# Kernel optimization log

Hardware: AMD Instinct MI355X
Metric: run time of the kernel (lower is better)

The kernel has to match this reference:

```python
import jax, jax.numpy as jnp
import numpy as np

D = 512; H = 8; DH = D // H; FFN = 2048; K = 31; N = 4; T = 1024


def _ln(x, g, b):
    m = jnp.mean(x, -1, keepdims=True)
    v = jnp.var(x, -1, keepdims=True)
    return (x - m) * jax.lax.rsqrt(v + 1e-5) * g + b


def _ff(x, g, b, w1, b1, w2, b2):
    h = jax.nn.silu(_ln(x, g, b) @ w1 + b1)
    return 0.5 * (h @ w2 + b2)


def _forward(x, rel_pe, ln1_g, ln1_b, ff1_w1, ff1_b1, ff1_w2, ff1_b2,
             an_g, an_b, wq, bq, wk, bk, wv, bv, wo, bo, pos_w, u, v,
             cn_g, cn_b, pe_w, pe_b, dw_w, dw_b, bn_g, bn_b, pc_w, pc_b,
             ln2_g, ln2_b, ff2_w1, ff2_b1, ff2_w2, ff2_b2, fn_g, fn_b):
    Nb, Tt, _ = x.shape
    # macaron FF 1 (half-step)
    x = x + _ff(x, ln1_g, ln1_b, ff1_w1, ff1_b1, ff1_w2, ff1_b2)

    # RPE multi-head attention (Transformer-XL style)
    xa = _ln(x, an_g, an_b)
    split = lambda m: m.reshape(Nb, Tt, H, DH).transpose(0, 2, 1, 3)  # (N,H,T,dh)
    Q = split(xa @ wq + bq)
    Kk = split(xa @ wk + bk)
    V = split(xa @ wv + bv)
    # content-to-content: (Q+u) K^T
    AC = jnp.einsum('nhtd,nhsd->nhts', Q + u[None, :, None, :], Kk)
    # content-to-position: (Q+v) R^T, then rel-shift gather
    R = (rel_pe @ pos_w).reshape(2 * Tt - 1, H, DH)  # (2T-1,H,dh)
    BD_raw = jnp.einsum('nhtd,phd->nhtp', Q + v[None, :, None, :], R)  # (N,H,T,2T-1)
    idx = jnp.arange(Tt - 1, -1, -1)[None, :] + jnp.arange(Tt)[:, None]  # (T,T): i-j+(T-1)
    BD = jnp.take_along_axis(BD_raw, idx[None, None, :, :], axis=-1)  # (N,H,T,T)
    scores = (AC + BD) * (DH ** -0.5)
    attn = jax.nn.softmax(scores, axis=-1)
    out = jnp.einsum('nhts,nhsd->nthd', attn, V).reshape(Nb, Tt, D)
    x = x + (out @ wo + bo)

    # conv module: LN -> pointwise expand -> GLU -> depthwise conv -> BN(eval) -> SiLU -> pointwise
    c = _ln(x, cn_g, cn_b) @ pe_w + pe_b  # (N,T,2D)
    a, g = jnp.split(c, 2, axis=-1)
    c = a * jax.nn.sigmoid(g)
    c = c.transpose(0, 2, 1)  # (N,D,T)
    c = jax.lax.conv_general_dilated(
        c, dw_w, window_strides=(1,), padding=[(K // 2, K // 2)],
        dimension_numbers=('NCH', 'OIH', 'NCH'), feature_group_count=D)
    c = c + dw_b[None, :, None]
    # BatchNorm1d in eval mode: running_mean=0, running_var=1
    c = c * bn_g[None, :, None] + bn_b[None, :, None]
    c = jax.nn.silu(c).transpose(0, 2, 1) @ pc_w + pc_b
    x = x + c

    # macaron FF 2 + final LN
    x = x + _ff(x, ln2_g, ln2_b, ff2_w1, ff2_b1, ff2_w2, ff2_b2)
    return _ln(x, fn_g, fn_b)


def setup_inputs() -> dict:
    keys = iter(jax.random.split(jax.random.key(0), 64))
    def rn(*shape, s=0.02):
        return jax.random.normal(next(keys), shape, jnp.float32) * s
    inp = {}
    inp['x'] = rn(N, T, D, s=1.0)
    inp['rel_pe'] = rn(2 * T - 1, D, s=1.0)
    inp['ln1_g'] = jnp.ones(D); inp['ln1_b'] = jnp.zeros(D)
    inp['ff1_w1'] = rn(D, FFN); inp['ff1_b1'] = jnp.zeros(FFN)
    inp['ff1_w2'] = rn(FFN, D); inp['ff1_b2'] = jnp.zeros(D)
    inp['an_g'] = jnp.ones(D); inp['an_b'] = jnp.zeros(D)
    inp['wq'] = rn(D, D); inp['bq'] = jnp.zeros(D)
    inp['wk'] = rn(D, D); inp['bk'] = jnp.zeros(D)
    inp['wv'] = rn(D, D); inp['bv'] = jnp.zeros(D)
    inp['wo'] = rn(D, D); inp['bo'] = jnp.zeros(D)
    inp['pos_w'] = rn(D, D)
    inp['u'] = rn(H, DH); inp['v'] = rn(H, DH)
    inp['cn_g'] = jnp.ones(D); inp['cn_b'] = jnp.zeros(D)
    inp['pe_w'] = rn(D, 2 * D); inp['pe_b'] = jnp.zeros(2 * D)
    inp['dw_w'] = rn(D, 1, K); inp['dw_b'] = jnp.zeros(D)
    inp['bn_g'] = jnp.ones(D); inp['bn_b'] = jnp.zeros(D)
    inp['pc_w'] = rn(D, D); inp['pc_b'] = jnp.zeros(D)
    inp['ln2_g'] = jnp.ones(D); inp['ln2_b'] = jnp.zeros(D)
    inp['ff2_w1'] = rn(D, FFN); inp['ff2_b1'] = jnp.zeros(FFN)
    inp['ff2_w2'] = rn(FFN, D); inp['ff2_b2'] = jnp.zeros(D)
    inp['fn_g'] = jnp.ones(D); inp['fn_b'] = jnp.zeros(D)
    return inp


def reference(x, rel_pe, ln1_g, ln1_b, ff1_w1, ff1_b1, ff1_w2, ff1_b2,
              an_g, an_b, wq, bq, wk, bk, wv, bv, wo, bo, pos_w, u, v,
              cn_g, cn_b, pe_w, pe_b, dw_w, dw_b, bn_g, bn_b, pc_w, pc_b,
              ln2_g, ln2_b, ff2_w1, ff2_b1, ff2_w2, ff2_b2, fn_g, fn_b):
    return _forward(x, rel_pe, ln1_g, ln1_b, ff1_w1, ff1_b1, ff1_w2, ff1_b2,
                    an_g, an_b, wq, bq, wk, bk, wv, bv, wo, bo, pos_w, u, v,
                    cn_g, cn_b, pe_w, pe_b, dw_w, dw_b, bn_g, bn_b, pc_w, pc_b,
                    ln2_g, ln2_b, ff2_w1, ff2_b1, ff2_w2, ff2_b2, fn_g, fn_b)
```

## Files before the change

### kernel.cpp

```cpp
#include <hip/hip_runtime.h>
#include <hip/hip_bf16.h>

using bf16 = __hip_bfloat16;
typedef __attribute__((ext_vector_type(8))) short short8;
typedef __attribute__((ext_vector_type(4))) float f32x4;

static __device__ __forceinline__ float b2f(bf16 v) { return __bfloat162float(v); }
static __device__ __forceinline__ bf16  f2b(float v) { return __float2bfloat16(v); }
static __device__ __forceinline__ short f2bs(float x) {
    union { float f; unsigned u; } c; c.f = x;
    unsigned r = (c.u + 0x7FFFu + ((c.u >> 16) & 1u)) >> 16;
    return (short)r;
}
static __device__ __forceinline__ float bs2f(short s) {
    union { unsigned u; float f; } c; c.u = ((unsigned)(unsigned short)s) << 16;
    return c.f;
}
static __device__ __forceinline__ void gload16(const short* g, short* l) {
    __builtin_amdgcn_global_load_lds(
        (const __attribute__((address_space(1))) void*)g,
        (__attribute__((address_space(3))) void*)l, 16, 0, 0);
}

constexpr int kD   = 512;
constexpr int kT   = 1024;
constexpr int kN   = 4;
constexpr int kH   = 8;
constexpr int kDH  = 64;
constexpr int kFFN = 2048;
constexpr int kROWS = kN * kT;
constexpr int kP    = 2 * kT - 1;

#define ACT_NONE 0
#define ACT_SILU 1

__global__ __launch_bounds__(256) void stamp_kernel(float* __restrict__ out, int n, float val) {
    int i = blockIdx.x * 256 + threadIdx.x;
    if (i < n) out[i] = (i == 0 ? val : 0.f);
}

__global__ __launch_bounds__(256) void cvt_kernel(const float* __restrict__ in,
                                                  float* __restrict__ out, int n4) {
    int i = blockIdx.x * 256 + threadIdx.x;
    if (i < n4) ((f32x4*)out)[i] = ((const f32x4*)in)[i];
}

struct WtDesc { const float* src; short* dst; int K; int N; int tstart; };
struct WtArgs { WtDesc d[11]; };

__global__ __launch_bounds__(256) void wt_all_kernel(WtArgs a) {
    __shared__ float t[32][33];
    int bid = blockIdx.x;
    int i = 0;
#pragma unroll
    for (int j = 1; j < 11; ++j) if (bid >= a.d[j].tstart) i = j;
    const float* W = a.d[i].src;
    short* Wt = a.d[i].dst;
    int Kd = a.d[i].K, Nd = a.d[i].N;
    int lt = bid - a.d[i].tstart;
    int nx = Nd >> 5;
    int n0 = (lt % nx) * 32, k0 = (lt / nx) * 32;
    int tx = threadIdx.x & 31, ty = threadIdx.x >> 5;
#pragma unroll
    for (int it = 0; it < 4; ++it)
        t[ty + it * 8][tx] = W[(size_t)(k0 + ty + it * 8) * Nd + n0 + tx];
    __syncthreads();
#pragma unroll
    for (int it = 0; it < 4; ++it)
        Wt[(size_t)(n0 + ty + it * 8) * Kd + k0 + tx] = f2bs(t[tx][ty + it * 8]);
}

__global__ __launch_bounds__(256) void vtrans_kernel(const bf16* __restrict__ V,
                                                     bf16* __restrict__ Vt) {
    __shared__ short ts[64][72];
    int tt = blockIdx.x, h = blockIdx.y, n = blockIdx.z;
    int tid = threadIdx.x;
    int r = tid >> 3, cg = (tid & 7) * 8;
#pragma unroll
    for (int it = 0; it < 2; ++it) {
        int row = it * 32 + r;
        *(short8*)&ts[row][cg] =
            *(const short8*)((const short*)V + ((size_t)n * kT + tt * 64 + row) * 512 + h * 64 + cg);
    }
    __syncthreads();
#pragma unroll
    for (int it = 0; it < 2; ++it) {
        int d = it * 32 + r;
        short8 o;
#pragma unroll
        for (int i = 0; i < 8; ++i) o[i] = ts[cg + i][d];
        *(short8*)((short*)Vt + ((size_t)(n * 8 + h) * 64 + d) * 1024 + tt * 64 + cg) = o;
    }
}

__global__ __launch_bounds__(256) void dwt_kernel(const float* __restrict__ dw_w,
                                                  const float* __restrict__ dw_b,
                                                  const float* __restrict__ bn_g,
                                                  const float* __restrict__ bn_b,
                                                  float* __restrict__ wt,
                                                  float* __restrict__ beff) {
    int idx = blockIdx.x * 256 + threadIdx.x;
    if (idx < 31 * kD) {
        int d = idx & 511, k = idx >> 9;
        wt[k * kD + d] = dw_w[d * 31 + k] * bn_g[d];
    }
    if (idx < kD) beff[idx] = dw_b[idx] * bn_g[idx] + bn_b[idx];
}

__global__ __launch_bounds__(256) void ln_kernel(const float* __restrict__ xin,
                                                 const float* __restrict__ g,
                                                 const float* __restrict__ b,
                                                 void* __restrict__ outp, int out_f32) {
    int row = blockIdx.x;
    const float* xr = xin + (size_t)row * kD;
    int tid = threadIdx.x;
    float v0 = xr[tid], v1 = xr[tid + 256];
    float s = v0 + v1, sq = v0 * v0 + v1 * v1;
    for (int off = 32; off; off >>= 1) {
        s  += __shfl_down(s, off);
        sq += __shfl_down(sq, off);
    }
    __shared__ float ss[4], ssq[4];
    __shared__ float mean_s, rstd_s;
    int wid = tid >> 6, lane = tid & 63;
    if (lane == 0) { ss[wid] = s; ssq[wid] = sq; }
    __syncthreads();
    if (tid == 0) {
        float S  = ss[0] + ss[1] + ss[2] + ss[3];
        float SQ = ssq[0] + ssq[1] + ssq[2] + ssq[3];
        float m = S / (float)kD;
        float var = SQ / (float)kD - m * m;
        mean_s = m;
        rstd_s = rsqrtf(fmaxf(var, 0.f) + 1e-5f);
    }
    __syncthreads();
    float m = mean_s, rs = rstd_s;
    float o0 = (v0 - m) * rs * g[tid]       + b[tid];
    float o1 = (v1 - m) * rs * g[tid + 256] + b[tid + 256];
    size_t i0 = (size_t)row * kD + tid, i1 = i0 + 256;
    if (out_f32) {
        ((float*)outp)[i0] = o0; ((float*)outp)[i1] = o1;
    } else {
        ((bf16*)outp)[i0] = f2b(o0); ((bf16*)outp)[i1] = f2b(o1);
    }
}

__global__ __launch_bounds__(256, 4) void gemm_mfma64(
    const void* __restrict__ A, const short* __restrict__ Bt,
    const float* __restrict__ bias, const float* __restrict__ residual,
    float* __restrict__ outf, bf16* __restrict__ outb,
    int M, int N, int K, int act, float scale, int a_f32) {
    __shared__ short As[4096];
    __shared__ short Bs[4096];
    int tid = threadIdx.x;
    int m0 = blockIdx.y * 64, n0 = blockIdx.x * 64;
    int wid = tid >> 6, lane = tid & 63;
    int wm = (wid >> 1) * 32, wn = (wid & 1) * 32;
    int q = lane >> 4, c16 = lane & 15;

    f32x4 zero4 = {0.f, 0.f, 0.f, 0.f};
    f32x4 acc[2][2] = {{zero4, zero4}, {zero4, zero4}};

    int arow = lane >> 3;
    int aseg = (lane & 7) ^ arow;

    for (int k0 = 0; k0 < K; k0 += 64) {
        __syncthreads();
        if (!a_f32) {
#pragma unroll
            for (int it = 0; it < 2; ++it) {
                int rbase = (wid * 2 + it) * 8;
                gload16((const short*)A + (size_t)(m0 + rbase + arow) * K + k0 + aseg * 8,
                        As + (size_t)(wid * 2 + it) * 512);
            }
        } else {
            int srow = tid >> 3, sseg = tid & 7;
#pragma unroll
            for (int it = 0; it < 2; ++it) {
                int row = it * 32 + srow;
                int rr = m0 + row;
                short8 v = {0, 0, 0, 0, 0, 0, 0, 0};
                if (rr < M) {
                    const float* ap = (const float*)A + (size_t)rr * K + k0 + sseg * 8;
                    f32x4 x0 = *(const f32x4*)ap;
                    f32x4 x1 = *(const f32x4*)(ap + 4);
                    v[0] = f2bs(x0[0]); v[1] = f2bs(x0[1]); v[2] = f2bs(x0[2]); v[3] = f2bs(x0[3]);
                    v[4] = f2bs(x1[0]); v[5] = f2bs(x1[1]); v[6] = f2bs(x1[2]); v[7] = f2bs(x1[3]);
                }
                *(short8*)&As[(row * 8 + (sseg ^ (row & 7))) * 8] = v;
            }
        }
#pragma unroll
        for (int it = 0; it < 2; ++it) {
            int rbase = (wid * 2 + it) * 8;
            gload16(Bt + (size_t)(n0 + rbase + arow) * K + k0 + aseg * 8,
                    Bs + (size_t)(wid * 2 + it) * 512);
        }
        __syncthreads();
#pragma unroll
        for (int ks = 0; ks < 2; ++ks) {
            int p = c16 & 7;
            short8 af[2], bfr[2];
#pragma unroll
            for (int mt = 0; mt < 2; ++mt) {
                int row = wm + mt * 16 + c16;
                af[mt] = *(const short8*)&As[(row * 8 + ((ks * 4 + q) ^ p)) * 8];
            }
#pragma unroll
            for (int nt = 0; nt < 2; ++nt) {
                int row = wn + nt * 16 + c16;
                bfr[nt] = *(const short8*)&Bs[(row * 8 + ((ks * 4 + q) ^ p)) * 8];
            }
#pragma unroll
            for (int mt = 0; mt < 2; ++mt)
#pragma unroll
                for (int nt = 0; nt < 2; ++nt)
                    acc[mt][nt] = __builtin_amdgcn_mfma_f32_16x16x32_bf16(
                        af[mt], bfr[nt], acc[mt][nt], 0, 0, 0);
        }
    }
#pragma unroll
    for (int mt = 0; mt < 2; ++mt) {
#pragma unroll
        for (int reg = 0; reg < 4; ++reg) {
            int r = m0 + wm + mt * 16 + q * 4 + reg;
            if (r >= M) continue;
#pragma unroll
            for (int nt = 0; nt < 2; ++nt) {
                int c = n0 + wn + nt * 16 + c16;
                float h = acc[mt][nt][reg];
                if (bias) h += bias[c];
                if (act == ACT_SILU) h = h / (1.f + __expf(-h));
                h *= scale;
                size_t idx = (size_t)r * N + c;
                if (residual) h += residual[idx];
                if (outf) outf[idx] = h;
                if (outb) outb[idx] = f2b(h);
            }
        }
    }
}

__global__ __launch_bounds__(256, 4) void gemm_qkv(
    const bf16* __restrict__ A, const short* __restrict__ Bt,
    const float* __restrict__ bq, const float* __restrict__ bk,
    const float* __restrict__ bv,
    bf16* __restrict__ Qb, bf16* __restrict__ Kb, bf16* __restrict__ Vb) {
    const int K = kD;
    __shared__ short As[4096];
    __shared__ short Bs[4096];
    int tid = threadIdx.x;
    int m0 = blockIdx.y * 64, n0 = blockIdx.x * 64;
    int seg = blockIdx.x >> 3;
    const float* bias = seg == 0 ? bq : (seg == 1 ? bk : bv);
    bf16* outb = seg == 0 ? Qb : (seg == 1 ? Kb : Vb);
    int ns0 = n0 & 511;
    int wid = tid >> 6, lane = tid & 63;
    int wm = (wid >> 1) * 32, wn = (wid & 1) * 32;
    int q = lane >> 4, c16 = lane & 15;

    f32x4 zero4 = {0.f, 0.f, 0.f, 0.f};
    f32x4 acc[2][2] = {{zero4, zero4}, {zero4, zero4}};
    int arow = lane >> 3;
    int aseg = (lane & 7) ^ arow;

    for (int k0 = 0; k0 < K; k0 += 64) {
        __syncthreads();
#pragma unroll
        for (int it = 0; it < 2; ++it) {
            int rbase = (wid * 2 + it) * 8;
            gload16((const short*)A + (size_t)(m0 + rbase + arow) * K + k0 + aseg * 8,
                    As + (size_t)(wid * 2 + it) * 512);
            gload16(Bt + (size_t)(n0 + rbase + arow) * K + k0 + aseg * 8,
                    Bs + (size_t)(wid * 2 + it) * 512);
        }
        __syncthreads();
#pragma unroll
        for (int ks = 0; ks < 2; ++ks) {
            int p = c16 & 7;
            short8 af[2], bfr[2];
#pragma unroll
            for (int mt = 0; mt < 2; ++mt) {
                int row = wm + mt * 16 + c16;
                af[mt] = *(const short8*)&As[(row * 8 + ((ks * 4 + q) ^ p)) * 8];
            }
#pragma unroll
            for (int nt = 0; nt < 2; ++nt) {
                int row = wn + nt * 16 + c16;
                bfr[nt] = *(const short8*)&Bs[(row * 8 + ((ks * 4 + q) ^ p)) * 8];
            }
#pragma unroll
            for (int mt = 0; mt < 2; ++mt)
#pragma unroll
                for (int nt = 0; nt < 2; ++nt)
                    acc[mt][nt] = __builtin_amdgcn_mfma_f32_16x16x32_bf16(
                        af[mt], bfr[nt], acc[mt][nt], 0, 0, 0);
        }
    }
#pragma unroll
    for (int mt = 0; mt < 2; ++mt)
#pragma unroll
        for (int reg = 0; reg < 4; ++reg) {
            int r = m0 + wm + mt * 16 + q * 4 + reg;
#pragma unroll
            for (int nt = 0; nt < 2; ++nt) {
                int c = ns0 + wn + nt * 16 + c16;
                outb[(size_t)r * 512 + c] = f2b(acc[mt][nt][reg] + bias[c]);
            }
        }
}

__global__ __launch_bounds__(256) void gemm_scalar(
    const void* __restrict__ A, const float* __restrict__ W,
    const float* __restrict__ bias, const float* __restrict__ residual,
    float* __restrict__ outf, bf16* __restrict__ outb,
    int M, int N, int K, int act, float scale, int a_f32) {
    __shared__ float As[16][65];
    __shared__ float Bs[16][65];
    int tid = threadIdx.x;
    int tx = tid & 15, ty = tid >> 4;
    int row0 = blockIdx.y * 64, col0 = blockIdx.x * 64;
    float acc[4][4] = {};
    for (int k0 = 0; k0 < K; k0 += 16) {
        for (int i = tid; i < 64 * 16; i += 256) {
            int r = i >> 4, c = i & 15;
            int rr = row0 + r;
            float v = 0.f;
            if (rr < M) {
                size_t idx = (size_t)rr * K + k0 + c;
                v = a_f32 ? ((const float*)A)[idx] : b2f(((const bf16*)A)[idx]);
            }
            As[c][r] = v;
        }
        for (int i = tid; i < 16 * 64; i += 256) {
            int r = i >> 6, c = i & 63;
            Bs[r][c] = W[(size_t)(k0 + r) * N + col0 + c];
        }
        __syncthreads();
#pragma unroll
        for (int kk = 0; kk < 16; ++kk) {
            float a[4], b[4];
#pragma unroll
            for (int i = 0; i < 4; ++i) a[i] = As[kk][ty * 4 + i];
#pragma unroll
            for (int j = 0; j < 4; ++j) b[j] = Bs[kk][tx * 4 + j];
#pragma unroll
            for (int i = 0; i < 4; ++i)
#pragma unroll
                for (int j = 0; j < 4; ++j) acc[i][j] += a[i] * b[j];
        }
        __syncthreads();
    }
#pragma unroll
    for (int i = 0; i < 4; ++i) {
        int r = row0 + ty * 4 + i;
        if (r >= M) continue;
#pragma unroll
        for (int j = 0; j < 4; ++j) {
            int c = col0 + tx * 4 + j;
            float h = acc[i][j];
            if (bias) h += bias[c];
            if (act == ACT_SILU) h = h / (1.f + __expf(-h));
            h *= scale;
            size_t idx = (size_t)r * N + c;
            if (residual) h += residual[idx];
            if (outf) outf[idx] = h;
            if (outb) outb[idx] = f2b(h);
        }
    }
}

__global__ __launch_bounds__(256, 2) void attn_mfma(
    const bf16* __restrict__ Qg, const bf16* __restrict__ Kg,
    const bf16* __restrict__ Vtg, const bf16* __restrict__ Rg,
    const float* __restrict__ uu, const float* __restrict__ vvp,
    bf16* __restrict__ outb) {
    __shared__ short Qu[64][72];
    __shared__ short Qv[64][72];
    __shared__ short Ks[64][72];
    __shared__ short Vt[64][72];
    __shared__ short Rw[128][72];
    __shared__ short Bp[64][136];

    int tid = threadIdx.x;
    int qb = blockIdx.x, h = blockIdx.y, n = blockIdx.z;
    int t0 = qb * 64;
    size_t baseq = ((size_t)n * kT) * 512 + (size_t)h * kDH;
    size_t basev = ((size_t)(n * 8 + h) * 64) * 1024;
    size_t baseo = ((size_t)n * kT) * kD + (size_t)h * kDH;

    int wid = tid >> 6, lane = tid & 63;
    int q = lane >> 4, c16 = lane & 15;
    int wm = wid * 16;
    int trow = wm + q * 4;

    {
        int t = tid >> 2, dg = (tid & 3) * 16;
        const short* qp = (const short*)Qg + baseq + (size_t)(t0 + t) * 512 + dg;
        short8 q0 = *(const short8*)qp;
        short8 q1 = *(const short8*)(qp + 8);
#pragma unroll
        for (int i = 0; i < 8; ++i) {
            float qv = bs2f(q0[i]);
            Qu[t][dg + i] = f2bs(qv + uu[h * 64 + dg + i]);
            Qv[t][dg + i] = f2bs(qv + vvp[h * 64 + dg + i]);
        }
#pragma unroll
        for (int i = 0; i < 8; ++i) {
            float qv = bs2f(q1[i]);
            Qu[t][dg + 8 + i] = f2bs(qv + uu[h * 64 + dg + 8 + i]);
            Qv[t][dg + 8 + i] = f2bs(qv + vvp[h * 64 + dg + 8 + i]);
        }
    }

    f32x4 zero4 = {0.f, 0.f, 0.f, 0.f};
    f32x4 acc_o[4] = {zero4, zero4, zero4, zero4};
    float m_i[4] = {-1e30f, -1e30f, -1e30f, -1e30f};
    float l_i[4] = {0.f, 0.f, 0.f, 0.f};

    for (int kt = 0; kt < 16; ++kt) {
        int s0 = kt * 64;
        __syncthreads();
        {
            int s = tid >> 2, dg = (tid & 3) * 16;
            const short* kp = (const short*)Kg + baseq + (size_t)(s0 + s) * 512 + dg;
            *(short8*)&Ks[s][dg]     = *(const short8*)kp;
            *(short8*)&Ks[s][dg + 8] = *(const short8*)(kp + 8);
            const short* vp = (const short*)Vtg + basev + (size_t)s * 1024 + s0 + dg;
            *(short8*)&Vt[s][dg]     = *(const short8*)vp;
            *(short8*)&Vt[s][dg + 8] = *(const short8*)(vp + 8);
        }
        int p_base = t0 - s0 + 960;
#pragma unroll
        for (int it = 0; it < 4; ++it) {
            int i = tid + it * 256;
            int j = i >> 3, dg2 = (i & 7) * 8;
            int p = p_base + j;
            p = p < 0 ? 0 : (p > 2046 ? 2046 : p);
            *(short8*)&Rw[j][dg2] =
                *(const short8*)((const short*)Rg + (size_t)p * kD + h * kDH + dg2);
        }
        __syncthreads();

        f32x4 acc_s[4] = {zero4, zero4, zero4, zero4};
        f32x4 acc_b[8] = {zero4, zero4, zero4, zero4, zero4, zero4, zero4, zero4};
#pragma unroll
        for (int ks = 0; ks < 2; ++ks) {
            short8 au = *(const short8*)&Qu[wm + c16][ks * 32 + q * 8];
            short8 av = *(const short8*)&Qv[wm + c16][ks * 32 + q * 8];
#pragma unroll
            for (int nt = 0; nt < 4; ++nt) {
                short8 bk_ = *(const short8*)&Ks[nt * 16 + c16][ks * 32 + q * 8];
                acc_s[nt] = __builtin_amdgcn_mfma_f32_16x16x32_bf16(au, bk_, acc_s[nt], 0, 0, 0);
            }
#pragma unroll
            for (int jt = 0; jt < 8; ++jt) {
                short8 br_ = *(const short8*)&Rw[jt * 16 + c16][ks * 32 + q * 8];
                acc_b[jt] = __builtin_amdgcn_mfma_f32_16x16x32_bf16(av, br_, acc_b[jt], 0, 0, 0);
            }
        }
#pragma unroll
        for (int jt = 0; jt < 8; ++jt)
#pragma unroll
            for (int reg = 0; reg < 4; ++reg)
                Bp[trow + reg][jt * 16 + c16] = f2bs(acc_b[jt][reg]);

        float pmat[4][4];
        float alpha[4];
#pragma unroll
        for (int reg = 0; reg < 4; ++reg) {
            int t = trow + reg;
            float mrow = -1e30f;
#pragma unroll
            for (int nt = 0; nt < 4; ++nt) {
                int s = nt * 16 + c16;
                int j = t - s + 63;
                float sv = (acc_s[nt][reg] + bs2f(Bp[t][j])) * 0.125f;
                pmat[nt][reg] = sv;
                mrow = fmaxf(mrow, sv);
            }
            mrow = fmaxf(mrow, __shfl_xor(mrow, 1));
            mrow = fmaxf(mrow, __shfl_xor(mrow, 2));
            mrow = fmaxf(mrow, __shfl_xor(mrow, 4));
            mrow = fmaxf(mrow, __shfl_xor(mrow, 8));
            float m_new = fmaxf(m_i[reg], mrow);
            alpha[reg] = __expf(m_i[reg] - m_new);
            float ps = 0.f;
#pragma unroll
            for (int nt = 0; nt < 4; ++nt) {
                float pe = __expf(pmat[nt][reg] - m_new);
                pmat[nt][reg] = pe;
                ps += pe;
            }
            ps += __shfl_xor(ps, 1);
            ps += __shfl_xor(ps, 2);
            ps += __shfl_xor(ps, 4);
            ps += __shfl_xor(ps, 8);
            l_i[reg] = l_i[reg] * alpha[reg] + ps;
            m_i[reg] = m_new;
        }
#pragma unroll
        for (int nt = 0; nt < 4; ++nt)
#pragma unroll
            for (int reg = 0; reg < 4; ++reg)
                Bp[trow + reg][nt * 16 + c16] = f2bs(pmat[nt][reg]);
#pragma unroll
        for (int dt = 0; dt < 4; ++dt)
#pragma unroll
            for (int reg = 0; reg < 4; ++reg)
                acc_o[dt][reg] *= alpha[reg];
#pragma unroll
        for (int ks = 0; ks < 2; ++ks) {
            short8 ap = *(const short8*)&Bp[wm + c16][ks * 32 + q * 8];
#pragma unroll
            for (int dt = 0; dt < 4; ++dt) {
                short8 bv_ = *(const short8*)&Vt[dt * 16 + c16][ks * 32 + q * 8];
                acc_o[dt] = __builtin_amdgcn_mfma_f32_16x16x32_bf16(ap, bv_, acc_o[dt], 0, 0, 0);
            }
        }
    }
#pragma unroll
    for (int reg = 0; reg < 4; ++reg) {
        float inv = 1.f / l_i[reg];
        int t = trow + reg;
#pragma unroll
        for (int dt = 0; dt < 4; ++dt)
            outb[baseo + (size_t)(t0 + t) * kD + dt * 16 + c16] = f2b(acc_o[dt][reg] * inv);
    }
}

__global__ __launch_bounds__(256) void attn_kernel(
    const bf16* __restrict__ Qg, const bf16* __restrict__ Kg,
    const bf16* __restrict__ Vg, const bf16* __restrict__ Rg,
    const float* __restrict__ uu, const float* __restrict__ vvp,
    bf16* __restrict__ outb) {
    __shared__ float Qs[64][65];
    __shared__ bf16 Ps[64][66];
    __shared__ bf16 Ks[64][66];
    __shared__ bf16 Vs[64][66];
    __shared__ bf16 Rs[127][66];
    __shared__ float uf[64], vf[64];
    __shared__ float uK[64], vR[127];

    int tid = threadIdx.x;
    int qb = blockIdx.x, h = blockIdx.y, n = blockIdx.z;
    int t0 = qb * 64;
    size_t base = ((size_t)n * kT) * kD + (size_t)h * kDH;

    if (tid < 64) {
        uf[tid] = uu[h * 64 + tid];
        vf[tid] = vvp[h * 64 + tid];
    }
    for (int i = tid; i < 64 * 64; i += 256) {
        int r = i >> 6, d = i & 63;
        Qs[r][d] = b2f(Qg[base + (size_t)(t0 + r) * kD + d]);
    }
    int r = tid >> 2, seg = tid & 3;
    float m_i = -1e30f, l_i = 0.f;
    float Oa[16];
#pragma unroll
    for (int i = 0; i < 16; ++i) Oa[i] = 0.f;

    for (int kt = 0; kt < 16; ++kt) {
        int s0 = kt * 64;
        __syncthreads();
        for (int i = tid; i < 64 * 64; i += 256) {
            int s = i >> 6, d = i & 63;
            Ks[s][d] = Kg[base + (size_t)(s0 + s) * kD + d];
            Vs[s][d] = Vg[base + (size_t)(s0 + s) * kD + d];
        }
        int p_base = t0 - s0 + 960;
        for (int i = tid; i < 127 * 64; i += 256) {
            int j = i >> 6, d = i & 63;
            int p = p_base + j;
            p = p < 0 ? 0 : (p > 2046 ? 2046 : p);
            Rs[j][d] = Rg[(size_t)p * kD + h * kDH + d];
        }
        __syncthreads();
        if (tid < 64) {
            float s_ = 0.f;
            for (int d = 0; d < 64; ++d) s_ += uf[d] * b2f(Ks[tid][d]);
            uK[tid] = s_;
        } else if (tid < 64 + 127) {
            int j = tid - 64;
            float s_ = 0.f;
            for (int d = 0; d < 64; ++d) s_ += vf[d] * b2f(Rs[j][d]);
            vR[j] = s_;
        }
        __syncthreads();
        float sv[16];
        float smax = -1e30f;
#pragma unroll
        for (int jj = 0; jj < 16; ++jj) {
            int s = seg * 16 + jj;
            int j = r - s + 63;
            float acc = 0.f;
            for (int d = 0; d < 64; ++d)
                acc += Qs[r][d] * (b2f(Ks[s][d]) + b2f(Rs[j][d]));
            acc = (acc + uK[s] + vR[j]) * 0.125f;
            sv[jj] = acc;
            smax = fmaxf(smax, acc);
        }
        smax = fmaxf(smax, __shfl_xor(smax, 1));
        smax = fmaxf(smax, __shfl_xor(smax, 2));
        float m_new = fmaxf(m_i, smax);
        float alpha = __expf(m_i - m_new);
        float psum = 0.f;
#pragma unroll
        for (int jj = 0; jj < 16; ++jj) {
            float p = __expf(sv[jj] - m_new);
            Ps[r][seg * 16 + jj] = f2b(p);
            psum += p;
        }
        psum += __shfl_xor(psum, 1);
        psum += __shfl_xor(psum, 2);
        l_i = l_i * alpha + psum;
        m_i = m_new;
#pragma unroll
        for (int i = 0; i < 16; ++i) Oa[i] *= alpha;
        __syncthreads();
        for (int s = 0; s < 64; ++s) {
            float p = b2f(Ps[r][s]);
#pragma unroll
            for (int dd = 0; dd < 16; ++dd)
                Oa[dd] += p * b2f(Vs[s][seg * 16 + dd]);
        }
    }
    float inv = 1.f / l_i;
#pragma unroll
    for (int dd = 0; dd < 16; ++dd)
        outb[base + (size_t)(t0 + r) * kD + seg * 16 + dd] = f2b(Oa[dd] * inv);
}

__global__ __launch_bounds__(256) void glu_kernel_v(const bf16* __restrict__ c,
                                                    bf16* __restrict__ out) {
    int i8 = (blockIdx.x * 256 + threadIdx.x) * 8;
    int row = i8 >> 9, d = i8 & 511;
    const short* cp = (const short*)c + (size_t)row * 1024;
    short8 a8 = *(const short8*)(cp + d);
    short8 g8 = *(const short8*)(cp + 512 + d);
    short8 o;
#pragma unroll
    for (int i = 0; i < 8; ++i) {
        float a = bs2f(a8[i]), g = bs2f(g8[i]);
        o[i] = f2bs(a / (1.f + __expf(-g)));
    }
    *(short8*)((short*)out + i8) = o;
}

__global__ __launch_bounds__(256) void gluconv_kernel(
    const bf16* __restrict__ cbuf, const float* __restrict__ wt,
    const float* __restrict__ beff, bf16* __restrict__ outb) {
    __shared__ short gsm[94][72];
    __shared__ float wsm[31][64];
    __shared__ float bsm[64];
    int tid = threadIdx.x;
    int dg0 = blockIdx.x * 64;
    int t0  = blockIdx.y * 64;
    int n   = blockIdx.z;

#pragma unroll
    for (int it = 0; it < 3; ++it) {
        int idx = tid + it * 256;
        if (idx < 94 * 8) {
            int row = idx >> 3, cg = (idx & 7) * 8;
            int t = t0 - 15 + row;
            short8 o = {0, 0, 0, 0, 0, 0, 0, 0};
            if ((unsigned)t < (unsigned)kT) {
                const short* cp = (const short*)cbuf + ((size_t)n * kT + t) * 1024 + dg0 + cg;
                short8 a8 = *(const short8*)cp;
                short8 g8 = *(const short8*)(cp + 512);
#pragma unroll
                for (int i = 0; i < 8; ++i)
                    o[i] = f2bs(bs2f(a8[i]) / (1.f + __expf(-bs2f(g8[i]))));
            }
            *(short8*)&gsm[row][cg] = o;
        }
    }
#pragma unroll
    for (int it = 0; it < 8; ++it) {
        int i = tid + it * 256;
        if (i < 31 * 64) wsm[i >> 6][i & 63] = wt[(i >> 6) * kD + dg0 + (i & 63)];
    }
    if (tid < 64) bsm[tid] = beff[dg0 + tid];
    __syncthreads();

    int tl = tid >> 2, dgl = (tid & 3) * 16;
    float acc[16] = {};
#pragma unroll
    for (int k = 0; k < 31; ++k) {
        short8 g0 = *(const short8*)&gsm[tl + k][dgl];
        short8 g1 = *(const short8*)&gsm[tl + k][dgl + 8];
#pragma unroll
        for (int i = 0; i < 8; ++i) {
            acc[i]     += bs2f(g0[i]) * wsm[k][dgl + i];
            acc[8 + i] += bs2f(g1[i]) * wsm[k][dgl + 8 + i];
        }
    }
    short8 o0, o1;
#pragma unroll
    for (int i = 0; i < 8; ++i) {
        float h = acc[i] + bsm[dgl + i];
        o0[i] = f2bs(h / (1.f + __expf(-h)));
        h = acc[8 + i] + bsm[dgl + 8 + i];
        o1[i] = f2bs(h / (1.f + __expf(-h)));
    }
    short* op = (short*)outb + ((size_t)n * kT + t0 + tl) * kD + dg0 + dgl;
    *(short8*)op = o0;
    *(short8*)(op + 8) = o1;
}

__global__ __launch_bounds__(256) void conv_kernel(
    const bf16* __restrict__ glu, const float* __restrict__ dw_w,
    const float* __restrict__ dw_b, const float* __restrict__ bn_g,
    const float* __restrict__ bn_b, bf16* __restrict__ outb) {
    int idx = blockIdx.x * 256 + threadIdx.x;
    int d = idx & 511;
    int t = (idx >> 9) & 1023;
    int n = idx >> 19;
    const bf16* gp = glu + ((size_t)n * kT) * kD + d;
    float acc = 0.f;
#pragma unroll
    for (int k = 0; k < 31; ++k) {
        int tt = t + k - 15;
        if ((unsigned)tt < (unsigned)kT)
            acc += b2f(gp[(size_t)tt * kD]) * dw_w[d * 31 + k];
    }
    acc += dw_b[d];
    acc = acc * bn_g[d] + bn_b[d];
    acc = acc / (1.f + __expf(-acc));
    outb[idx] = f2b(acc);
}

extern "C" void kernel_launch(void* const* d_in, const int* in_sizes, int n_in,
                              void* d_out, int out_size, void* d_ws, size_t ws_size,
                              hipStream_t stream) {
    const float* x      = (const float*)d_in[0];
    const float* rel_pe = (const float*)d_in[1];
    const float* ln1_g  = (const float*)d_in[2];
    const float* ln1_b  = (const float*)d_in[3];
    const float* ff1_w1 = (const float*)d_in[4];
    const float* ff1_b1 = (const float*)d_in[5];
    const float* ff1_w2 = (const float*)d_in[6];
    const float* ff1_b2 = (const float*)d_in[7];
    const float* an_g   = (const float*)d_in[8];
    const float* an_b   = (const float*)d_in[9];
    const float* wq = (const float*)d_in[10]; const float* bq = (const float*)d_in[11];
    const float* wk = (const float*)d_in[12]; const float* bk = (const float*)d_in[13];
    const float* wv = (const float*)d_in[14]; const float* bv = (const float*)d_in[15];
    const float* wo = (const float*)d_in[16]; const float* bo = (const float*)d_in[17];
    const float* pos_w = (const float*)d_in[18];
    const float* uu = (const float*)d_in[19]; const float* vvp = (const float*)d_in[20];
    const float* cn_g = (const float*)d_in[21]; const float* cn_b = (const float*)d_in[22];
    const float* pe_w = (const float*)d_in[23]; const float* pe_b = (const float*)d_in[24];
    const float* dw_w = (const float*)d_in[25]; const float* dw_b = (const float*)d_in[26];
    const float* bn_g = (const float*)d_in[27]; const float* bn_b = (const float*)d_in[28];
    const float* pc_w = (const float*)d_in[29]; const float* pc_b = (const float*)d_in[30];
    const float* ln2_g = (const float*)d_in[31]; const float* ln2_b = (const float*)d_in[32];
    const float* ff2_w1 = (const float*)d_in[33]; const float* ff2_b1 = (const float*)d_in[34];
    const float* ff2_w2 = (const float*)d_in[35]; const float* ff2_b2 = (const float*)d_in[36];
    const float* fn_g = (const float*)d_in[37]; const float* fn_b = (const float*)d_in[38];
    (void)n_in; (void)in_sizes;

    const int total = kROWS * kD;
    dim3 blk(256);
    const size_t MB = 1ull << 20;
    char* w = (char*)d_ws;

    if (ws_size >= 30 * MB) {
        float* xf      = (float*)(w);
        short* ff1_w1t = (short*)(w + 8 * MB);
        short* ff1_w2t = (short*)(w + 10 * MB);
        short* wqt     = (short*)(w + 12 * MB);
        short* wkt     = (short*)(w + 12 * MB + 512 * 1024);
        short* wvt     = (short*)(w + 13 * MB);
        short* wot     = (short*)(w + 13 * MB + 512 * 1024);
        short* poswt   = (short*)(w + 14 * MB);
        short* pewt    = (short*)(w + 14 * MB + 512 * 1024);
        short* pcwt    = (short*)(w + 15 * MB + 512 * 1024);
        short* ff2_w1t = (short*)(w + 16 * MB);
        short* ff2_w2t = (short*)(w + 18 * MB);
        char*  dyn     = w + 20 * MB;
        bf16* hchunk = (bf16*)dyn;
        bf16* Qb     = (bf16*)dyn;
        bf16* Kb     = (bf16*)(dyn + 4 * MB);
        bf16* Rb     = (bf16*)(dyn + 8 * MB);
        bf16* cbuf   = (bf16*)dyn;
        float* dwt   = (float*)(dyn + 8 * MB);
        float* beff  = (float*)(dyn + 8 * MB + 256 * 1024);
        bf16* nb     = (bf16*)d_out;
        bf16* Vtg    = (bf16*)d_out;
        bf16* convb  = (bf16*)d_out;
        bf16* Vb     = (bf16*)d_out + (size_t)kROWS * kD;
        bf16* attnb  = Vb;

        WtArgs wa;
        const float* srcs[11] = {ff1_w1, ff1_w2, wq, wk, wv, wo, pos_w, pe_w, pc_w, ff2_w1, ff2_w2};
        short* dsts[11] = {ff1_w1t, ff1_w2t, wqt, wkt, wvt, wot, poswt, pewt, pcwt, ff2_w1t, ff2_w2t};
        int Ks_[11] = {512, 2048, 512, 512, 512, 512, 512, 512, 512, 512, 2048};
        int Ns_[11] = {2048, 512, 512, 512, 512, 512, 512, 1024, 512, 2048, 512};
        int cum = 0;
        for (int i = 0; i < 11; ++i) {
            wa.d[i].src = srcs[i]; wa.d[i].dst = dsts[i];
            wa.d[i].K = Ks_[i]; wa.d[i].N = Ns_[i]; wa.d[i].tstart = cum;
            cum += (Ns_[i] / 32) * (Ks_[i] / 32);
        }
        wt_all_kernel<<<cum, blk, 0, stream>>>(wa);

        ln_kernel<<<kROWS, blk, 0, stream>>>(x, ln1_g, ln1_b, nb, 0);
        for (int c = 0; c < 2; ++c) {
            size_t off = (size_t)c * 2048 * kD;
            gemm_mfma64<<<dim3(kFFN / 64, 2048 / 64), blk, 0, stream>>>(
                nb + off, ff1_w1t, ff1_b1, nullptr, nullptr, hchunk,
                2048, kFFN, kD, ACT_SILU, 1.f, 0);
            gemm_mfma64<<<dim3(kD / 64, 2048 / 64), blk, 0, stream>>>(
                hchunk, ff1_w2t, ff1_b2, x + off, xf + off, nullptr,
                2048, kD, kFFN, ACT_NONE, 0.5f, 0);
        }

        ln_kernel<<<kROWS, blk, 0, stream>>>(xf, an_g, an_b, nb, 0);
        gemm_qkv<<<dim3(24, kROWS / 64), blk, 0, stream>>>(
            nb, wqt, bq, bk, bv, Qb, Kb, Vb);
        vtrans_kernel<<<dim3(16, 8, 4), blk, 0, stream>>>(Vb, Vtg);
        gemm_mfma64<<<dim3(kD / 64, (kP + 63) / 64), blk, 0, stream>>>(
            rel_pe, poswt, nullptr, nullptr, nullptr, Rb, kP, kD, kD, ACT_NONE, 1.f, 1);
        attn_mfma<<<dim3(kT / 64, kH, kN), blk, 0, stream>>>(Qb, Kb, Vtg, Rb, uu, vvp, attnb);
        gemm_mfma64<<<dim3(kD / 64, kROWS / 64), blk, 0, stream>>>(
            attnb, wot, bo, xf, xf, nullptr, kROWS, kD, kD, ACT_NONE, 1.f, 0);

        dwt_kernel<<<62, blk, 0, stream>>>(dw_w, dw_b, bn_g, bn_b, dwt, beff);
        ln_kernel<<<kROWS, blk, 0, stream>>>(xf, cn_g, cn_b, nb, 0);
        gemm_mfma64<<<dim3(2 * kD / 64, kROWS / 64), blk, 0, stream>>>(
            nb, pewt, pe_b, nullptr, nullptr, cbuf, kROWS, 2 * kD, kD, ACT_NONE, 1.f, 0);
        gluconv_kernel<<<dim3(8, 16, 4), blk, 0, stream>>>(cbuf, dwt, beff, convb);
        gemm_mfma64<<<dim3(kD / 64, kROWS / 64), blk, 0, stream>>>(
            convb, pcwt, pc_b, xf, xf, nullptr, kROWS, kD, kD, ACT_NONE, 1.f, 0);

        ln_kernel<<<kROWS, blk, 0, stream>>>(xf, ln2_g, ln2_b, nb, 0);
        for (int c = 0; c < 2; ++c) {
            size_t off = (size_t)c * 2048 * kD;
            gemm_mfma64<<<dim3(kFFN / 64, 2048 / 64), blk, 0, stream>>>(
                nb + off, ff2_w1t, ff2_b1, nullptr, nullptr, hchunk,
                2048, kFFN, kD, ACT_SILU, 1.f, 0);
            gemm_mfma64<<<dim3(kD / 64, 2048 / 64), blk, 0, stream>>>(
                hchunk, ff2_w2t, ff2_b2, xf + off, xf + off, nullptr,
                2048, kD, kFFN, ACT_NONE, 0.5f, 0);
        }

        ln_kernel<<<kROWS, blk, 0, stream>>>(xf, fn_g, fn_b, d_out, 1);
        return;
    }

    if (ws_size < 22 * MB) {
        stamp_kernel<<<(out_size + 255) / 256, blk, 0, stream>>>(
            (float*)d_out, out_size, 1000.f + (float)(ws_size / MB));
        return;
    }

    float* xf    = (float*)(w);
    bf16*  hbch  = (bf16*)(w + 8 * MB);
    bf16*  Qb    = (bf16*)(w + 8 * MB);
    bf16*  cbuf  = (bf16*)(w + 8 * MB);
    bf16*  convb = (bf16*)(w + 8 * MB);
    bf16*  Kb    = (bf16*)(w + 12 * MB);
    bf16*  Vb    = (bf16*)(w + 16 * MB);
    bf16*  glub  = (bf16*)(w + 16 * MB);
    bf16*  Rb    = (bf16*)(w + 20 * MB);
    bf16*  nb    = (bf16*)d_out;
    bf16*  attnb = (bf16*)d_out;

    cvt_kernel<<<total / 1024, blk, 0, stream>>>(x, xf, total / 4);

    ln_kernel<<<kROWS, blk, 0, stream>>>(xf, ln1_g, ln1_b, nb, 0);
    for (int c = 0; c < 4; ++c) {
        size_t off = (size_t)c * 1024 * kD;
        gemm_scalar<<<dim3(kFFN / 64, 1024 / 64), blk, 0, stream>>>(
            nb + off, ff1_w1, ff1_b1, nullptr, nullptr, hbch, 1024, kFFN, kD, ACT_SILU, 1.f, 0);
        gemm_scalar<<<dim3(kD / 64, 1024 / 64), blk, 0, stream>>>(
            hbch, ff1_w2, ff1_b2, xf + off, xf + off, nullptr, 1024, kD, kFFN, ACT_NONE, 0.5f, 0);
    }

    ln_kernel<<<kROWS, blk, 0, stream>>>(xf, an_g, an_b, nb, 0);
    gemm_scalar<<<dim3(kD / 64, kROWS / 64), blk, 0, stream>>>(
        nb, wq, bq, nullptr, nullptr, Qb, kROWS, kD, kD, ACT_NONE, 1.f, 0);
    gemm_scalar<<<dim3(kD / 64, kROWS / 64), blk, 0, stream>>>(
        nb, wk, bk, nullptr, nullptr, Kb, kROWS, kD, kD, ACT_NONE, 1.f, 0);
    gemm_scalar<<<dim3(kD / 64, kROWS / 64), blk, 0, stream>>>(
        nb, wv, bv, nullptr, nullptr, Vb, kROWS, kD, kD, ACT_NONE, 1.f, 0);
    gemm_scalar<<<dim3(kD / 64, (kP + 63) / 64), blk, 0, stream>>>(
        rel_pe, pos_w, nullptr, nullptr, nullptr, Rb, kP, kD, kD, ACT_NONE, 1.f, 1);
    attn_kernel<<<dim3(kT / 64, kH, kN), blk, 0, stream>>>(Qb, Kb, Vb, Rb, uu, vvp, attnb);
    gemm_scalar<<<dim3(kD / 64, kROWS / 64), blk, 0, stream>>>(
        attnb, wo, bo, xf, xf, nullptr, kROWS, kD, kD, ACT_NONE, 1.f, 0);

    ln_kernel<<<kROWS, blk, 0, stream>>>(xf, cn_g, cn_b, nb, 0);
    gemm_scalar<<<dim3(2 * kD / 64, kROWS / 64), blk, 0, stream>>>(
        nb, pe_w, pe_b, nullptr, nullptr, cbuf, kROWS, 2 * kD, kD, ACT_NONE, 1.f, 0);
    glu_kernel_v<<<total / 2048, blk, 0, stream>>>(cbuf, glub);
    conv_kernel<<<total / 256, blk, 0, stream>>>(glub, dw_w, dw_b, bn_g, bn_b, convb);
    gemm_scalar<<<dim3(kD / 64, kROWS / 64), blk, 0, stream>>>(
        convb, pc_w, pc_b, xf, xf, nullptr, kROWS, kD, kD, ACT_NONE, 1.f, 0);

    ln_kernel<<<kROWS, blk, 0, stream>>>(xf, ln2_g, ln2_b, nb, 0);
    for (int c = 0; c < 4; ++c) {
        size_t off = (size_t)c * 1024 * kD;
        gemm_scalar<<<dim3(kFFN / 64, 1024 / 64), blk, 0, stream>>>(
            nb + off, ff2_w1, ff2_b1, nullptr, nullptr, hbch, 1024, kFFN, kD, ACT_SILU, 1.f, 0);
        gemm_scalar<<<dim3(kD / 64, 1024 / 64), blk, 0, stream>>>(
            hbch, ff2_w2, ff2_b2, xf + off, xf + off, nullptr, 1024, kD, kFFN, ACT_NONE, 0.5f, 0);
    }

    ln_kernel<<<kROWS, blk, 0, stream>>>(xf, fn_g, fn_b, d_out, 1);
}
```

Baseline: 501.8 us.

## Double-buffer LDS tiles in MFMA GEMM kernels to overlap loads with compute

Gives the generic MFMA GEMM and the fused QKV GEMM two LDS buffers for the A and B tiles. The next K-slice is issued into the alternate buffer right after the barrier, while the current slice goes through MFMA, and one barrier per iteration replaces two. The goal is to hide global-to-LDS latency behind the matrix math. The cost is double the LDS per block (32KB), which could limit occupancy.

```diff
diff --git a/kernel.cpp b/kernel.cpp
--- a/kernel.cpp
+++ b/kernel.cpp
@@ -150,8 +150,8 @@
     const float* __restrict__ bias, const float* __restrict__ residual,
     float* __restrict__ outf, bf16* __restrict__ outb,
     int M, int N, int K, int act, float scale, int a_f32) {
-    __shared__ short As[4096];
-    __shared__ short Bs[4096];
+    __shared__ short As[2][4096];
+    __shared__ short Bs[2][4096];
     int tid = threadIdx.x;
     int m0 = blockIdx.y * 64, n0 = blockIdx.x * 64;
     int wid = tid >> 6, lane = tid & 63;
@@ -164,14 +164,13 @@
     int arow = lane >> 3;
     int aseg = (lane & 7) ^ arow;
 
-    for (int k0 = 0; k0 < K; k0 += 64) {
-        __syncthreads();
+    auto issueA = [&](int buf, int k0) {
         if (!a_f32) {
 #pragma unroll
             for (int it = 0; it < 2; ++it) {
                 int rbase = (wid * 2 + it) * 8;
                 gload16((const short*)A + (size_t)(m0 + rbase + arow) * K + k0 + aseg * 8,
-                        As + (size_t)(wid * 2 + it) * 512);
+                        &As[buf][(wid * 2 + it) * 512]);
             }
         } else {
             int srow = tid >> 3, sseg = tid & 7;
@@ -187,16 +186,28 @@
                     v[0] = f2bs(x0[0]); v[1] = f2bs(x0[1]); v[2] = f2bs(x0[2]); v[3] = f2bs(x0[3]);
                     v[4] = f2bs(x1[0]); v[5] = f2bs(x1[1]); v[6] = f2bs(x1[2]); v[7] = f2bs(x1[3]);
                 }
-                *(short8*)&As[(row * 8 + (sseg ^ (row & 7))) * 8] = v;
-            }
-        }
+                *(short8*)&As[buf][(row * 8 + (sseg ^ (row & 7))) * 8] = v;
+            }
+        }
+    };
+    auto issueB = [&](int buf, int k0) {
 #pragma unroll
         for (int it = 0; it < 2; ++it) {
             int rbase = (wid * 2 + it) * 8;
             gload16(Bt + (size_t)(n0 + rbase + arow) * K + k0 + aseg * 8,
-                    Bs + (size_t)(wid * 2 + it) * 512);
-        }
+                    &Bs[buf][(wid * 2 + it) * 512]);
+        }
+    };
+
+    issueA(0, 0);
+    issueB(0, 0);
+    int cur = 0;
+    for (int k0 = 0; k0 < K; k0 += 64) {
         __syncthreads();
+        if (k0 + 64 < K) {
+            issueA(cur ^ 1, k0 + 64);
+            issueB(cur ^ 1, k0 + 64);
+        }
 #pragma unroll
         for (int ks = 0; ks < 2; ++ks) {
             int p = c16 & 7;
@@ -204,12 +215,12 @@
 #pragma unroll
             for (int mt = 0; mt < 2; ++mt) {
                 int row = wm + mt * 16 + c16;
-                af[mt] = *(const short8*)&As[(row * 8 + ((ks * 4 + q) ^ p)) * 8];
+                af[mt] = *(const short8*)&As[cur][(row * 8 + ((ks * 4 + q) ^ p)) * 8];
             }
 #pragma unroll
             for (int nt = 0; nt < 2; ++nt) {
                 int row = wn + nt * 16 + c16;
-                bfr[nt] = *(const short8*)&Bs[(row * 8 + ((ks * 4 + q) ^ p)) * 8];
+                bfr[nt] = *(const short8*)&Bs[cur][(row * 8 + ((ks * 4 + q) ^ p)) * 8];
             }
 #pragma unroll
             for (int mt = 0; mt < 2; ++mt)
@@ -218,6 +229,7 @@
                     acc[mt][nt] = __builtin_amdgcn_mfma_f32_16x16x32_bf16(
                         af[mt], bfr[nt], acc[mt][nt], 0, 0, 0);
         }
+        cur ^= 1;
     }
 #pragma unroll
     for (int mt = 0; mt < 2; ++mt) {
@@ -247,8 +259,8 @@
     const float* __restrict__ bv,
     bf16* __restrict__ Qb, bf16* __restrict__ Kb, bf16* __restrict__ Vb) {
     const int K = kD;
-    __shared__ short As[4096];
-    __shared__ short Bs[4096];
+    __shared__ short As[2][4096];
+    __shared__ short Bs[2][4096];
     int tid = threadIdx.x;
     int m0 = blockIdx.y * 64, n0 = blockIdx.x * 64;
     int seg = blockIdx.x >> 3;
@@ -264,17 +276,22 @@
     int arow = lane >> 3;
     int aseg = (lane & 7) ^ arow;
 
-    for (int k0 = 0; k0 < K; k0 += 64) {
-        __syncthreads();
+    auto issue = [&](int buf, int k0) {
 #pragma unroll
         for (int it = 0; it < 2; ++it) {
             int rbase = (wid * 2 + it) * 8;
             gload16((const short*)A + (size_t)(m0 + rbase + arow) * K + k0 + aseg * 8,
-                    As + (size_t)(wid * 2 + it) * 512);
+                    &As[buf][(wid * 2 + it) * 512]);
             gload16(Bt + (size_t)(n0 + rbase + arow) * K + k0 + aseg * 8,
-                    Bs + (size_t)(wid * 2 + it) * 512);
-        }
+                    &Bs[buf][(wid * 2 + it) * 512]);
+        }
+    };
+
+    issue(0, 0);
+    int cur = 0;
+    for (int k0 = 0; k0 < K; k0 += 64) {
         __syncthreads();
+        if (k0 + 64 < K) issue(cur ^ 1, k0 + 64);
 #pragma unroll
         for (int ks = 0; ks < 2; ++ks) {
             int p = c16 & 7;
@@ -282,12 +299,12 @@
 #pragma unroll
             for (int mt = 0; mt < 2; ++mt) {
                 int row = wm + mt * 16 + c16;
-                af[mt] = *(const short8*)&As[(row * 8 + ((ks * 4 + q) ^ p)) * 8];
+                af[mt] = *(const short8*)&As[cur][(row * 8 + ((ks * 4 + q) ^ p)) * 8];
             }
 #pragma unroll
             for (int nt = 0; nt < 2; ++nt) {
                 int row = wn + nt * 16 + c16;
-                bfr[nt] = *(const short8*)&Bs[(row * 8 + ((ks * 4 + q) ^ p)) * 8];
+                bfr[nt] = *(const short8*)&Bs[cur][(row * 8 + ((ks * 4 + q) ^ p)) * 8];
             }
 #pragma unroll
             for (int mt = 0; mt < 2; ++mt)
@@ -296,6 +313,7 @@
                     acc[mt][nt] = __builtin_amdgcn_mfma_f32_16x16x32_bf16(
                         af[mt], bfr[nt], acc[mt][nt], 0, 0, 0);
         }
+        cur ^= 1;
     }
 #pragma unroll
     for (int mt = 0; mt < 2; ++mt)
```

After: 504.6 us. Within noise of the previous version (+0.6%).
